# Optimization experiments

Hardware: AMD Instinct MI355X
Metric: run time of the kernel (lower is better)

## Reference

```python
import jax, jax.numpy as jnp
import numpy as np
from jax import lax

NB = 8        # nbands
BS = 32       # block_size
MTF = 41      # MTF kernel size
N = BS * BS   # self.N = block_size**2


def _dwconv(x, k):
    # depthwise (groups=NB) VALID conv, NCHW / OIHW
    return lax.conv_general_dilated(
        x, k, window_strides=(1, 1), padding='VALID',
        dimension_numbers=('NCHW', 'OIHW', 'NCHW'),
        feature_group_count=NB)


def setup_inputs() -> dict:
    key = jax.random.key(0)
    k1, k2, k3 = jax.random.split(key, 3)
    outputs = jax.random.normal(k1, (4, NB, 552, 552), dtype=jnp.float32)
    labels = jax.random.normal(k2, (4, NB, 512, 512), dtype=jnp.float32)
    # frozen per-band MTF lowpass kernel (requires_grad=False in the original)
    mtf_kernel = jax.random.normal(k3, (NB, 1, MTF, MTF), dtype=jnp.float32) * 0.02
    return {"outputs": outputs, "labels": labels, "mtf_kernel": mtf_kernel}


def reference(outputs, labels, mtf_kernel):
    box = jnp.ones((NB, 1, BS, BS), dtype=jnp.float32)  # all-ones box kernel
    o = _dwconv(outputs, mtf_kernel)                    # [4,NB,512,512]
    # five box-sum (moving window sum) maps -> [4,NB,481,481]
    o_sum = _dwconv(o, box)
    l_sum = _dwconv(labels, box)
    o_sq_sum = _dwconv(o * o, box)
    l_sq_sum = _dwconv(labels * labels, box)
    ol_sum = _dwconv(o * labels, box)

    mul = o_sum * l_sum                     # outputs_labels_sum_mul
    sq = o_sum ** 2 + l_sum ** 2            # outputs_labels_sum_mul_sq
    numerator = 4.0 * (N * ol_sum - mul) * mul
    denom_temp = N * (o_sq_sum + l_sq_sum) - sq
    denominator = denom_temp * sq

    quality_map = jnp.ones_like(denominator)
    idx1 = (denom_temp == 0) & (sq != 0)
    quality_map = jnp.where(idx1, 2.0 * mul / jnp.where(idx1, sq, 1.0), quality_map)
    idx2 = denominator != 0
    quality_map = jnp.where(idx2, numerator / jnp.where(idx2, denominator, 1.0), quality_map)

    return 1.0 - jnp.mean(quality_map)
```

## Files before the change

### kernel.cpp

```cpp
#include <hip/hip_runtime.h>

#define NBANDS 8
#define BS 32
#define MTF 41
#define IMG 552
#define CONV 512
#define QOUT 481
#define NIMG 32
#define NN 1024.0f
#define KXP 42

#define TX 560
#define TY 576

typedef _Float16 half8 __attribute__((ext_vector_type(8)));
typedef _Float16 half2v __attribute__((ext_vector_type(2)));
typedef float f32x16 __attribute__((ext_vector_type(16)));

__global__ __launch_bounds__(256) void prep_transpose(
    const float* __restrict__ in, _Float16* __restrict__ T)
{
    __shared__ _Float16 s[64][72];
    int bid = blockIdx.x;
    int img = bid / 81;
    int t = bid % 81;
    int ty = t / 9, tx2 = t % 9;
    int y0 = ty * 64, x0 = tx2 * 64;
    const float* ip = in + (size_t)img * IMG * IMG;

    for (int k = 0; k < 16; ++k) {
        int i = k * 256 + threadIdx.x;
        int r = i >> 6, c = i & 63;
        int y = y0 + r, x = x0 + c;
        float v = (y < IMG && x < IMG) ? ip[(size_t)y * IMG + x] : 0.f;
        s[c][r] = (_Float16)v;
    }
    __syncthreads();
    _Float16* Tp = T + (size_t)img * TX * TY;
    for (int k = 0; k < 2; ++k) {
        int i = k * 256 + threadIdx.x;
        int xi = i >> 3, g = i & 7;
        int x = x0 + xi;
        if (x < TX) {
            half8 v = *(const half8*)&s[xi][g * 8];
            *(half8*)&Tp[(size_t)x * TY + y0 + g * 8] = v;
        }
    }
}

__global__ __launch_bounds__(320) void prep_atab32(
    const float* __restrict__ w, _Float16* __restrict__ A)
{
    int bid = blockIdx.x;
    int band = bid / KXP, kx = bid % KXP;
    int s = threadIdx.x >> 6, lane = threadIdx.x & 63;
    int i = lane & 31;
    int kb = 16 * s + ((lane >> 5) << 3);
    const float* wp = w + band * MTF * MTF;
    half8 v;
#pragma unroll
    for (int j = 0; j < 8; ++j) {
        int ky = kb + j - i;
        v[j] = (kx < MTF && ky >= 0 && ky < MTF) ? (_Float16)wp[ky * MTF + kx]
                                                 : (_Float16)0.f;
    }
    *(half8*)&A[(((size_t)bid * 5 + s) << 9) + lane * 8] = v;
}

#define XP4 296
#define GSTR4 (2 * XP4 * 16)

__global__ __launch_bounds__(512, 2) void conv_mfma_512(
    const _Float16* __restrict__ T, const _Float16* __restrict__ Atab,
    float* __restrict__ out)
{
    extern __shared__ _Float16 sB[];
    int bid = blockIdx.x;
    int img = bid >> 3;
    int rr  = bid & 7;
    int yb  = rr >> 1, xb = rr & 1;
    int y0 = yb << 7;
    int x0 = xb << 8;
    int band = img & 7;
    int tid = threadIdx.x;

    const _Float16* Tp = T + (size_t)img * TX * TY;
    for (int e = tid; e < 22 * XP4; e += 512) {
        int g = e / XP4, x = e - g * XP4;
        half8 v = *(const half8*)&Tp[(size_t)(x0 + x) * TY + y0 + g * 8];
        *(half8*)&sB[(size_t)e * 8] = v;
    }
    __syncthreads();

    int l  = tid & 63;
    int wx = tid >> 6;
    int p  = l >> 5;
    int ln = l & 31;

    const half8* Ab = (const half8*)(Atab + (((size_t)band * KXP * 5) << 9)) + l;
    const char* bbase = (const char*)sB + ((size_t)(p * XP4 + (wx << 5) + ln) << 4);

    f32x16 acc0 = {}, acc1 = {}, acc2 = {}, acc3 = {};

    auto LDA = [&](half8 (&A)[5], int kx) {
        const half8* q = Ab + (size_t)kx * 5 * 64;
#pragma unroll
        for (int s = 0; s < 5; ++s) A[s] = q[(size_t)s * 64];
    };
    auto LDB = [&](half8 (&B)[11], int kx) {
        const char* q = bbase + ((size_t)kx << 4);
#pragma unroll
        for (int j = 0; j < 11; ++j) B[j] = *(const half8*)(q + j * GSTR4);
    };
    auto FMAS = [&](half8 (&A)[5], half8 (&B)[11]) {
#pragma unroll
        for (int s = 0; s < 5; ++s) {
            acc0 = __builtin_amdgcn_mfma_f32_32x32x16_f16(A[s], B[s],     acc0, 0, 0, 0);
            acc1 = __builtin_amdgcn_mfma_f32_32x32x16_f16(A[s], B[s + 2], acc1, 0, 0, 0);
            acc2 = __builtin_amdgcn_mfma_f32_32x32x16_f16(A[s], B[s + 4], acc2, 0, 0, 0);
            acc3 = __builtin_amdgcn_mfma_f32_32x32x16_f16(A[s], B[s + 6], acc3, 0, 0, 0);
        }
    };

    half8 A0[5], A1[5], B0[11], B1[11];
    LDA(A0, 0);
    LDA(A1, 1);
    LDB(B0, 0);
#pragma unroll 1
    for (int kx = 0; kx < 40; kx += 2) {
        LDB(B1, kx + 1);
        FMAS(A0, B0);
        LDA(A0, kx + 2);
        LDB(B0, kx + 2);
        FMAS(A1, B1);
        LDA(A1, kx + 3);
    }
    FMAS(A0, B0);

    float* op = out + (size_t)img * CONV * CONV;
    int colb = x0 + (wx << 5) + ln;
    int rb   = y0 + (p << 2);
#pragma unroll
    for (int r2 = 0; r2 < 16; ++r2) {
        int rowo = (r2 & 3) + ((r2 >> 2) << 3);
        op[(size_t)(rb + rowo) * CONV + colb]       = acc0[r2];
        op[(size_t)(rb + 32 + rowo) * CONV + colb]  = acc1[r2];
        op[(size_t)(rb + 64 + rowo) * CONV + colb]  = acc2[r2];
        op[(size_t)(rb + 96 + rowo) * CONV + colb]  = acc3[r2];
    }
}

template<int C, int RM, int BM, bool BC>
__device__ __forceinline__ int dppadd_h2(int v) {
    int t = __builtin_amdgcn_update_dpp(0, v, C, RM, BM, BC);
    half2v a = __builtin_bit_cast(half2v, v);
    half2v b = __builtin_bit_cast(half2v, t);
    return __builtin_bit_cast(int, a + b);
}

__device__ __forceinline__ int wave_iscan_h2(int v) {
    v = dppadd_h2<0x111, 0xf, 0xf, true >(v);
    v = dppadd_h2<0x112, 0xf, 0xf, true >(v);
    v = dppadd_h2<0x114, 0xf, 0xf, true >(v);
    v = dppadd_h2<0x118, 0xf, 0xf, true >(v);
    v = dppadd_h2<0x142, 0xa, 0xf, false>(v);
    v = dppadd_h2<0x143, 0xc, 0xf, false>(v);
    return v;
}

__device__ __forceinline__ void win32pair(float sa, float sb, int lane,
                                          float& wa, float& wb) {
    half2v p = __builtin_bit_cast(half2v, __builtin_amdgcn_cvt_pkrtz(sa, sb));
    int P = wave_iscan_h2(__builtin_bit_cast(int, p));
    int Pg = __shfl(P, lane + 31, 64);
    half2v w = __builtin_bit_cast(half2v, Pg) - __builtin_bit_cast(half2v, P) + p;
    wa = (float)w[0];
    wb = (float)w[1];
}

__device__ __forceinline__ float qval(float A0, float A1, float A2, float A3) {
    float mul = A0 * A1;
    float sq  = fmaf(A0, A0, A1 * A1);
    float num = 4.f * fmaf(NN, A3, -mul) * mul;
    float dt  = fmaf(NN, A2, -sq);
    float den = dt * sq;
    bool  c1  = (dt == 0.f) && (sq != 0.f);
    float nn = num, dd = den;
    if (den == 0.f) { nn = c1 ? 2.f * mul : 1.f; dd = c1 ? sq : 1.f; }
    return nn * __builtin_amdgcn_rcpf(dd);
}

#define B_OFF (31 * CONV)

__global__ __launch_bounds__(512) void box_q4(
    const float* __restrict__ o,
    const float* __restrict__ lab,
    double* __restrict__ acc)
{
    int bid  = blockIdx.x;
    int img  = bid >> 4;
    int rr   = bid & 15;
    int pair = rr >> 1;
    int xblk = rr & 1;
    int lane = threadIdx.x & 63;
    int wid  = threadIdx.x >> 6;

    int c0 = xblk * 256 + wid * 32;
    int cc = min(c0 + lane, CONV - 1);
    int r0A = pair * 62;

    const float* op = o   + (size_t)img * CONV * CONV + cc;
    const float* lp = lab + (size_t)img * CONV * CONV + cc;

    bool xvalid = (lane < 32) && (c0 + lane < QOUT);

    float sA0=0,sA1=0,sA2=0,sA3=0, sB0=0,sB1=0,sB2=0,sB3=0;
    {
        int ofs = r0A * CONV;
#pragma unroll 4
        for (int k = 0; k < BS; ++k) {
            float ov = op[ofs],         lv = lp[ofs];
            float ow = op[ofs + B_OFF], lw = lp[ofs + B_OFF];
            sA0 += ov; sA1 += lv;
            sA2 = fmaf(ov, ov, fmaf(lv, lv, sA2)); sA3 = fmaf(ov, lv, sA3);
            sB0 += ow; sB1 += lw;
            sB2 = fmaf(ow, ow, fmaf(lw, lw, sB2)); sB3 = fmaf(ow, lw, sB3);
            ofs += CONV;
        }
    }

    float qacc = 0.f;
    int iadd = (r0A + BS) * CONV;
    int isub = r0A * CONV;

    if (pair < 7) {
#pragma unroll 1
        for (int i = 0; i < 30; ++i) {
            float oa = op[iadd],         la2 = lp[iadd];
            float ob = op[isub],         lb  = lp[isub];
            float oc = op[iadd + B_OFF], lc  = lp[iadd + B_OFF];
            float od = op[isub + B_OFF], ld  = lp[isub + B_OFF];

            float A0, A1, A2, A3, B0, B1, B2, B3;
            win32pair(sA0, sA1, lane, A0, A1);
            win32pair(sA2, sA3, lane, A2, A3);
            win32pair(sB0, sB1, lane, B0, B1);
            win32pair(sB2, sB3, lane, B2, B3);
            if (xvalid) {
                qacc += qval(A0, A1, A2, A3);
                qacc += qval(B0, B1, B2, B3);
            }

            sA0 += oa - ob; sA1 += la2 - lb;
            sA2 = fmaf(oa, oa, fmaf(la2, la2, fmaf(ob, -ob, fmaf(lb, -lb, sA2))));
            sA3 = fmaf(oa, la2, fmaf(ob, -lb, sA3));
            sB0 += oc - od; sB1 += lc - ld;
            sB2 = fmaf(oc, oc, fmaf(lc, lc, fmaf(od, -od, fmaf(ld, -ld, sB2))));
            sB3 = fmaf(oc, lc, fmaf(od, -ld, sB3));
            iadd += CONV; isub += CONV;
        }
        {
            float A0, A1, A2, A3, B0, B1, B2, B3;
            win32pair(sA0, sA1, lane, A0, A1);
            win32pair(sA2, sA3, lane, A2, A3);
            win32pair(sB0, sB1, lane, B0, B1);
            win32pair(sB2, sB3, lane, B2, B3);
            if (xvalid) {
                qacc += qval(A0, A1, A2, A3);
                qacc += qval(B0, B1, B2, B3);
            }
        }
    } else {
#pragma unroll 1
        for (int i = 0; i < 31; ++i) {
            bool mA = (i < 30), mB = (i + 1 < 16);
            float oa=0,la2=0,ob=0,lb=0, oc=0,lc=0,od=0,ld=0;
            if (mA) {
                oa = op[iadd]; la2 = lp[iadd];
                ob = op[isub]; lb  = lp[isub];
            }
            if (mB) {
                oc = op[iadd + B_OFF]; lc = lp[iadd + B_OFF];
                od = op[isub + B_OFF]; ld = lp[isub + B_OFF];
            }

            {
                float A0, A1, A2, A3;
                win32pair(sA0, sA1, lane, A0, A1);
                win32pair(sA2, sA3, lane, A2, A3);
                if (xvalid) qacc += qval(A0, A1, A2, A3);
            }
            if (i < 16) {
                float B0, B1, B2, B3;
                win32pair(sB0, sB1, lane, B0, B1);
                win32pair(sB2, sB3, lane, B2, B3);
                if (xvalid) qacc += qval(B0, B1, B2, B3);
            }

            sA0 += oa - ob; sA1 += la2 - lb;
            sA2 = fmaf(oa, oa, fmaf(la2, la2, fmaf(ob, -ob, fmaf(lb, -lb, sA2))));
            sA3 = fmaf(oa, la2, fmaf(ob, -lb, sA3));
            sB0 += oc - od; sB1 += lc - ld;
            sB2 = fmaf(oc, oc, fmaf(lc, lc, fmaf(od, -od, fmaf(ld, -ld, sB2))));
            sB3 = fmaf(oc, lc, fmaf(od, -ld, sB3));
            iadd += CONV; isub += CONV;
        }
    }

    qacc += __shfl_down(qacc, 16, 64);
    qacc += __shfl_down(qacc, 8, 64);
    qacc += __shfl_down(qacc, 4, 64);
    qacc += __shfl_down(qacc, 2, 64);
    qacc += __shfl_down(qacc, 1, 64);
    if (lane == 0) atomicAdd(&acc[img], (double)qacc);
}

__global__ void finalize_kernel(const double* __restrict__ acc, float* __restrict__ out)
{
    double t = 0.0;
    for (int i = 0; i < NIMG; ++i) t += acc[i];
    out[0] = 1.0f - (float)(t / 7403552.0);
}

extern "C" void kernel_launch(void* const* d_in, const int* in_sizes, int n_in,
                              void* d_out, int out_size, void* d_ws, size_t ws_size,
                              hipStream_t stream)
{
    const float* outputs = (const float*)d_in[0];
    const float* labels  = (const float*)d_in[1];
    const float* mtf     = (const float*)d_in[2];

    double*    acc   = (double*)d_ws;
    float*     o_buf = (float*)((char*)d_ws + 4096);
    _Float16*  T     = (_Float16*)((char*)d_ws + 4096 + 33554432);
    _Float16*  Atab  = (_Float16*)((char*)d_ws + 4096 + 33554432 + 20643840);

    (void)hipFuncSetAttribute((const void*)conv_mfma_512,
                              hipFuncAttributeMaxDynamicSharedMemorySize,
                              22 * XP4 * 16);

    hipMemsetAsync(d_ws, 0, 256, stream);

    prep_transpose<<<NIMG * 81, 256, 0, stream>>>(outputs, T);
    prep_atab32<<<NBANDS * KXP, 320, 0, stream>>>(mtf, Atab);
    conv_mfma_512<<<NIMG * 8, 512, 22 * XP4 * 16, stream>>>(T, Atab, o_buf);
    box_q4<<<NIMG * 16, 512, 0, stream>>>(o_buf, labels, acc);
    finalize_kernel<<<1, 1, 0, stream>>>(acc, (float*)d_out);
}
```

Before: 130.6 us.

## Switch MTF convolution to 16x16x32 MFMA with smaller tiles and more blocks

The Toeplitz-style MTF convolution moves from 32x32x16 MFMA tiles to 16x16x32 MFMA. Each block now covers a 128x64 output tile with 256 threads instead of 128x256 with 512, so there are four times as many blocks and the LDS footprint per block is smaller. The weight table is rebuilt for the 16-row layout, and the B register double-buffering is dropped in favour of a single buffer. This should raise occupancy and spread work more evenly across CUs, at the cost of more redundant halo loads into LDS and less overlap between loads and MFMAs.

```diff
diff --git a/kernel.cpp b/kernel.cpp
--- a/kernel.cpp
+++ b/kernel.cpp
@@ -15,7 +15,7 @@
 
 typedef _Float16 half8 __attribute__((ext_vector_type(8)));
 typedef _Float16 half2v __attribute__((ext_vector_type(2)));
-typedef float f32x16 __attribute__((ext_vector_type(16)));
+typedef float f32x4 __attribute__((ext_vector_type(4)));
 
 __global__ __launch_bounds__(256) void prep_transpose(
     const float* __restrict__ in, _Float16* __restrict__ T)
@@ -48,14 +48,14 @@
     }
 }
 
-__global__ __launch_bounds__(320) void prep_atab32(
+__global__ __launch_bounds__(128) void prep_atab16(
     const float* __restrict__ w, _Float16* __restrict__ A)
 {
     int bid = blockIdx.x;
     int band = bid / KXP, kx = bid % KXP;
     int s = threadIdx.x >> 6, lane = threadIdx.x & 63;
-    int i = lane & 31;
-    int kb = 16 * s + ((lane >> 5) << 3);
+    int i = lane & 15;
+    int kb = 32 * s + ((lane >> 4) << 3);
     const float* wp = w + band * MTF * MTF;
     half8 v;
 #pragma unroll
@@ -64,89 +64,83 @@
         v[j] = (kx < MTF && ky >= 0 && ky < MTF) ? (_Float16)wp[ky * MTF + kx]
                                                  : (_Float16)0.f;
     }
-    *(half8*)&A[(((size_t)bid * 5 + s) << 9) + lane * 8] = v;
-}
-
-#define XP4 296
-#define GSTR4 (2 * XP4 * 16)
-
-__global__ __launch_bounds__(512, 2) void conv_mfma_512(
+    *(half8*)&A[(((size_t)(bid * 2 + s)) << 9) + lane * 8] = v;
+}
+
+#define XP5 105
+#define UGS (2 * XP5 * 16)
+
+__global__ __launch_bounds__(256, 4) void conv_mfma16(
     const _Float16* __restrict__ T, const _Float16* __restrict__ Atab,
     float* __restrict__ out)
 {
-    extern __shared__ _Float16 sB[];
+    __shared__ __align__(16) _Float16 sB[22 * XP5 * 8];
     int bid = blockIdx.x;
-    int img = bid >> 3;
-    int rr  = bid & 7;
-    int yb  = rr >> 1, xb = rr & 1;
-    int y0 = yb << 7;
-    int x0 = xb << 8;
+    int img = bid >> 5;
+    int rr  = bid & 31;
+    int y0 = (rr >> 3) << 7;
+    int x0 = (rr & 7) << 6;
     int band = img & 7;
     int tid = threadIdx.x;
 
     const _Float16* Tp = T + (size_t)img * TX * TY;
-    for (int e = tid; e < 22 * XP4; e += 512) {
-        int g = e / XP4, x = e - g * XP4;
+    for (int e = tid; e < 22 * 104; e += 256) {
+        int g = e / 104, x = e - g * 104;
         half8 v = *(const half8*)&Tp[(size_t)(x0 + x) * TY + y0 + g * 8];
-        *(half8*)&sB[(size_t)e * 8] = v;
+        *(half8*)&sB[(size_t)(g * XP5 + x) * 8] = v;
     }
     __syncthreads();
 
     int l  = tid & 63;
     int wx = tid >> 6;
-    int p  = l >> 5;
-    int ln = l & 31;
-
-    const half8* Ab = (const half8*)(Atab + (((size_t)band * KXP * 5) << 9)) + l;
-    const char* bbase = (const char*)sB + ((size_t)(p * XP4 + (wx << 5) + ln) << 4);
-
-    f32x16 acc0 = {}, acc1 = {}, acc2 = {}, acc3 = {};
-
-    auto LDA = [&](half8 (&A)[5], int kx) {
-        const half8* q = Ab + (size_t)kx * 5 * 64;
-#pragma unroll
-        for (int s = 0; s < 5; ++s) A[s] = q[(size_t)s * 64];
+    int g4 = l >> 4;
+    int ln = l & 15;
+
+    const half8* Ab = (const half8*)Atab + (size_t)band * KXP * 2 * 64 + l;
+    const char* bbase = (const char*)sB + ((size_t)(g4 * XP5 + (wx << 4) + ln) << 4);
+
+    f32x4 acc[8] = {};
+
+    auto LDA = [&](half8 (&A)[2], int kx) {
+        A[0] = Ab[(size_t)(kx * 2) * 64];
+        A[1] = Ab[(size_t)(kx * 2 + 1) * 64];
     };
-    auto LDB = [&](half8 (&B)[11], int kx) {
+    auto LDB = [&](half8 (&B)[10], int kx) {
         const char* q = bbase + ((size_t)kx << 4);
 #pragma unroll
-        for (int j = 0; j < 11; ++j) B[j] = *(const half8*)(q + j * GSTR4);
+        for (int i = 0; i < 10; ++i) B[i] = *(const half8*)(q + i * UGS);
     };
-    auto FMAS = [&](half8 (&A)[5], half8 (&B)[11]) {
-#pragma unroll
-        for (int s = 0; s < 5; ++s) {
-            acc0 = __builtin_amdgcn_mfma_f32_32x32x16_f16(A[s], B[s],     acc0, 0, 0, 0);
-            acc1 = __builtin_amdgcn_mfma_f32_32x32x16_f16(A[s], B[s + 2], acc1, 0, 0, 0);
-            acc2 = __builtin_amdgcn_mfma_f32_32x32x16_f16(A[s], B[s + 4], acc2, 0, 0, 0);
-            acc3 = __builtin_amdgcn_mfma_f32_32x32x16_f16(A[s], B[s + 6], acc3, 0, 0, 0);
-        }
+    auto FMAS = [&](half8 (&A)[2], half8 (&B)[10]) {
+#pragma unroll
+        for (int t = 0; t < 8; ++t)
+            acc[t] = __builtin_amdgcn_mfma_f32_16x16x32_f16(A[0], B[t], acc[t], 0, 0, 0);
+#pragma unroll
+        for (int t = 0; t < 8; ++t)
+            acc[t] = __builtin_amdgcn_mfma_f32_16x16x32_f16(A[1], B[t + 2], acc[t], 0, 0, 0);
     };
 
-    half8 A0[5], A1[5], B0[11], B1[11];
+    half8 A0[2], A1[2], B[10];
     LDA(A0, 0);
-    LDA(A1, 1);
-    LDB(B0, 0);
 #pragma unroll 1
     for (int kx = 0; kx < 40; kx += 2) {
-        LDB(B1, kx + 1);
-        FMAS(A0, B0);
+        LDB(B, kx);
+        LDA(A1, kx + 1);
+        FMAS(A0, B);
+        LDB(B, kx + 1);
         LDA(A0, kx + 2);
-        LDB(B0, kx + 2);
-        FMAS(A1, B1);
-        LDA(A1, kx + 3);
-    }
-    FMAS(A0, B0);
+        FMAS(A1, B);
+    }
+    LDB(B, 40);
+    FMAS(A0, B);
 
     float* op = out + (size_t)img * CONV * CONV;
-    int colb = x0 + (wx << 5) + ln;
-    int rb   = y0 + (p << 2);
-#pragma unroll
-    for (int r2 = 0; r2 < 16; ++r2) {
-        int rowo = (r2 & 3) + ((r2 >> 2) << 3);
-        op[(size_t)(rb + rowo) * CONV + colb]       = acc0[r2];
-        op[(size_t)(rb + 32 + rowo) * CONV + colb]  = acc1[r2];
-        op[(size_t)(rb + 64 + rowo) * CONV + colb]  = acc2[r2];
-        op[(size_t)(rb + 96 + rowo) * CONV + colb]  = acc3[r2];
+    int col = x0 + (wx << 4) + ln;
+    int rb  = y0 + (g4 << 2);
+#pragma unroll
+    for (int t = 0; t < 8; ++t) {
+#pragma unroll
+        for (int r = 0; r < 4; ++r)
+            op[(size_t)(rb + 16 * t + r) * CONV + col] = acc[t][r];
     }
 }
 
@@ -335,15 +329,11 @@
     _Float16*  T     = (_Float16*)((char*)d_ws + 4096 + 33554432);
     _Float16*  Atab  = (_Float16*)((char*)d_ws + 4096 + 33554432 + 20643840);
 
-    (void)hipFuncSetAttribute((const void*)conv_mfma_512,
-                              hipFuncAttributeMaxDynamicSharedMemorySize,
-                              22 * XP4 * 16);
-
     hipMemsetAsync(d_ws, 0, 256, stream);
 
     prep_transpose<<<NIMG * 81, 256, 0, stream>>>(outputs, T);
-    prep_atab32<<<NBANDS * KXP, 320, 0, stream>>>(mtf, Atab);
-    conv_mfma_512<<<NIMG * 8, 512, 22 * XP4 * 16, stream>>>(T, Atab, o_buf);
+    prep_atab16<<<NBANDS * KXP, 128, 0, stream>>>(mtf, Atab);
+    conv_mfma16<<<NIMG * 32, 256, 0, stream>>>(T, Atab, o_buf);
     box_q4<<<NIMG * 16, 512, 0, stream>>>(o_buf, labels, acc);
     finalize_kernel<<<1, 1, 0, stream>>>(acc, (float*)d_out);
 }
```

Result: faster. 120.4 us (-7.8%).
